# Optimization experiments

Measured on AMD Instinct MI355X. Metric: run time of the kernel, lower is better.

The kernel has to match this reference:

```python
import jax, jax.numpy as jnp
import numpy as np

U_NUM = 100000
I_NUM = 50000
D = 64
E = 4_000_000
N_LAYERS = 3


def setup_inputs() -> dict:
    key = jax.random.key(0)
    k1, k2, k3, k4 = jax.random.split(key, 4)
    return {
        "user_emb": jax.random.normal(k1, (U_NUM + 1, D), dtype=jnp.float32) * 0.1,
        "item_emb": jax.random.normal(k2, (I_NUM + 1, D), dtype=jnp.float32) * 0.1,
        "edge_user": jax.random.randint(k3, (E,), 0, U_NUM + 1, dtype=jnp.int32),
        "edge_item": jax.random.randint(k4, (E,), 0, I_NUM + 1, dtype=jnp.int32),
    }


def reference(user_emb, item_emb, edge_user, edge_item):
    U = user_emb.shape[0]
    I = item_emb.shape[0]
    N = U + I
    # Symmetrize bipartite interaction edges into full-graph COO indices.
    rows = jnp.concatenate([edge_user, edge_item + U])          # [2E]
    cols = jnp.concatenate([edge_item + U, edge_user])          # [2E]
    # Symmetric degree normalization: A_hat = D^-1/2 A D^-1/2 (deg + 1e-7)
    deg = jax.ops.segment_sum(jnp.ones(rows.shape[0], dtype=jnp.float32), rows, num_segments=N) + 1e-7
    d_inv_sqrt = deg ** -0.5
    vals = d_inv_sqrt[rows] * d_inv_sqrt[cols]                  # [2E]

    emb = jnp.concatenate([user_emb, item_emb], axis=0)         # [N, D]
    acc = emb
    x = emb
    for _ in range(N_LAYERS):
        # SpMM: x_new[r] = sum_{edges (r,c)} vals * x[c]
        x = jax.ops.segment_sum(vals[:, None] * x[cols], rows, num_segments=N)
        acc = acc + x
    total = acc / jnp.float32(N_LAYERS + 1)                     # mean over layer stack
    return total[:U], total[U:]
```

## Files before the change

kernel.cpp:

```cpp
#include <hip/hip_runtime.h>


static constexpr int D = 64;
#define BSHIFT 8
#define BROWS 256
#define KP 1024
#define TILE 2048
#define PADSLACK (7 * BROWS)

__device__ __forceinline__ float bflo(unsigned v) {
    unsigned u = v << 16;
    return __builtin_bit_cast(float, u);
}
__device__ __forceinline__ float bfhi(unsigned v) {
    unsigned u = v & 0xFFFF0000u;
    return __builtin_bit_cast(float, u);
}
__device__ __forceinline__ unsigned pack_bf16x2(float a, float b) {
    unsigned ua = __builtin_bit_cast(unsigned, a);
    unsigned ub = __builtin_bit_cast(unsigned, b);
    ua += 0x7FFFu + ((ua >> 16) & 1u);
    ub += 0x7FFFu + ((ub >> 16) & 1u);
    return (ua >> 16) | (ub & 0xFFFF0000u);
}

__global__ __launch_bounds__(256) void bucket_count(
        const int* __restrict__ eu, const int* __restrict__ ei,
        int* __restrict__ bcnt, int E, int U) {
    __shared__ int h[KP];
    int tid = threadIdx.x;
#pragma unroll
    for (int k = 0; k < 4; ++k) h[tid + k * 256] = 0;
    __syncthreads();
    int E4 = E >> 2;
    int stride = gridDim.x * blockDim.x;
    int g = blockIdx.x * blockDim.x + tid;
    const int4* eu4 = (const int4*)eu;
    const int4* ei4 = (const int4*)ei;
    for (int e = g; e < E4; e += stride) {
        int4 u = eu4[e];
        int4 it = ei4[e];
        atomicAdd(&h[u.x >> BSHIFT], 1);
        atomicAdd(&h[u.y >> BSHIFT], 1);
        atomicAdd(&h[u.z >> BSHIFT], 1);
        atomicAdd(&h[u.w >> BSHIFT], 1);
        atomicAdd(&h[(U + it.x) >> BSHIFT], 1);
        atomicAdd(&h[(U + it.y) >> BSHIFT], 1);
        atomicAdd(&h[(U + it.z) >> BSHIFT], 1);
        atomicAdd(&h[(U + it.w) >> BSHIFT], 1);
    }
    if (blockIdx.x == 0 && tid < (E - (E4 << 2))) {
        int e = (E4 << 2) + tid;
        atomicAdd(&h[eu[e] >> BSHIFT], 1);
        atomicAdd(&h[(U + ei[e]) >> BSHIFT], 1);
    }
    __syncthreads();
#pragma unroll
    for (int k = 0; k < 4; ++k) {
        int v = h[tid + k * 256];
        if (v) atomicAdd(&bcnt[tid + k * 256], v);
    }
}

__global__ void bscan(const int* __restrict__ bcnt, int* __restrict__ bbase,
                      int* __restrict__ bcursor, int KB, int twoE) {
    __shared__ int s[KP];
    int tid = threadIdx.x;
    int v = (tid < KB) ? bcnt[tid] : 0;
    s[tid] = v;
    __syncthreads();
    for (int off = 1; off < KP; off <<= 1) {
        int a = (tid >= off) ? s[tid - off] : 0;
        __syncthreads();
        s[tid] += a;
        __syncthreads();
    }
    int ex = s[tid] - v;
    if (tid < KB) { bbase[tid] = ex; bcursor[tid] = ex; }
    if (tid == KB) bbase[tid] = twoE;
    if (tid > KB) bcursor[tid] = 0;
}

__global__ __launch_bounds__(256) void bucket_scatter(
        const int* __restrict__ eu, const int* __restrict__ ei,
        int* __restrict__ bcursor, unsigned* __restrict__ pairs,
        int E, int U, int twoE) {
    __shared__ int hist[KP];
    __shared__ int sbase[KP];
    __shared__ int gbase[KP];
    __shared__ unsigned staging[TILE];
    __shared__ unsigned short sb[TILE];
    int tid = threadIdx.x;
#pragma unroll
    for (int k = 0; k < 4; ++k) hist[tid + k * 256] = 0;
    __syncthreads();
    int base_e = blockIdx.x * TILE;
    int bk[8]; unsigned pk[8];
#pragma unroll
    for (int k = 0; k < 8; ++k) {
        int e = base_e + k * 256 + tid;
        bk[k] = -1;
        if (e < twoE) {
            int r, c;
            if (e < E) { r = eu[e]; c = U + ei[e]; }
            else       { c = eu[e - E]; r = U + ei[e - E]; }
            int b = r >> BSHIFT;
            bk[k] = b;
            pk[k] = ((unsigned)(r & (BROWS - 1)) << 18) | (unsigned)c;
            atomicAdd(&hist[b], 1);
        }
    }
    __syncthreads();
    int cc[4];
#pragma unroll
    for (int k = 0; k < 4; ++k) cc[k] = hist[tid + k * 256];
    for (int off = 1; off < KP; off <<= 1) {
        int a[4];
#pragma unroll
        for (int k = 0; k < 4; ++k) {
            int idx = tid + k * 256;
            a[k] = (idx >= off) ? hist[idx - off] : 0;
        }
        __syncthreads();
#pragma unroll
        for (int k = 0; k < 4; ++k) hist[tid + k * 256] += a[k];
        __syncthreads();
    }
#pragma unroll
    for (int k = 0; k < 4; ++k) {
        int idx = tid + k * 256;
        int e0 = hist[idx] - cc[k];
        sbase[idx] = e0;
        if (cc[k] > 0) gbase[idx] = atomicAdd(&bcursor[idx], cc[k]);
        hist[idx] = e0;
    }
    __syncthreads();
#pragma unroll
    for (int k = 0; k < 8; ++k) {
        if (bk[k] >= 0) {
            int pos = atomicAdd(&hist[bk[k]], 1);
            staging[pos] = pk[k];
            sb[pos] = (unsigned short)bk[k];
        }
    }
    __syncthreads();
    int tile_n = min(TILE, twoE - base_e);
#pragma unroll
    for (int k = 0; k < 8; ++k) {
        int j = k * 256 + tid;
        if (j < tile_n) {
            int b = sb[j];
            pairs[gbase[b] + (j - sbase[b])] = staging[j];
        }
    }
}

__global__ __launch_bounds__(256) void csr_build(
        const unsigned* __restrict__ pairs, const int* __restrict__ bbase,
        int* __restrict__ deg, int* __restrict__ row_ptr, float* __restrict__ dis,
        int* __restrict__ cols, int N) {
    __shared__ int cnt[BROWS];
    __shared__ int cur[BROWS];
    __shared__ int fin[BROWS];
    int tid = threadIdx.x;
    int b = blockIdx.x;
    int lo = bbase[b], hi = bbase[b + 1];
    int cbase = lo + PADSLACK * b;
    cnt[tid] = 0;
    __syncthreads();
    for (int i = lo + tid; i < hi; i += 256) atomicAdd(&cnt[pairs[i] >> 18], 1);
    __syncthreads();
    int c = cnt[tid];
    int p = (c + 7) & ~7;
    cnt[tid] = p;
    __syncthreads();
    for (int off = 1; off < BROWS; off <<= 1) {
        int a = (tid >= off) ? cnt[tid - off] : 0;
        __syncthreads();
        cnt[tid] += a;
        __syncthreads();
    }
    int e = cnt[tid] - p;
    int r = (b << BSHIFT) + tid;
    if (r < N) {
        deg[r] = c;
        row_ptr[r] = cbase + e;
        dis[r] = rsqrtf((float)c + 1e-7f);
    }
    cur[tid] = e;
    fin[tid] = e + p;
    __syncthreads();
    for (int i = lo + tid; i < hi; i += 256) {
        unsigned pe = pairs[i];
        int pos = atomicAdd(&cur[pe >> 18], 1);
        cols[cbase + pos] = (int)(pe & 0x3FFFFu);
    }
    __syncthreads();
    for (int i = cur[tid]; i < fin[tid]; ++i) cols[cbase + i] = N;
}

__global__ __launch_bounds__(256) void init_kernel(
        const float4* __restrict__ ue4, const float4* __restrict__ ie4,
        const float* __restrict__ dis,
        uint4* __restrict__ xsA4, uint4* __restrict__ xsB4,
        float4* __restrict__ acc4, int U8, int N8) {
    int t = blockIdx.x * blockDim.x + threadIdx.x;
    if (t >= N8 + 8) return;
    if (t >= N8) {
        uint4 z = {0u, 0u, 0u, 0u};
        xsA4[t] = z;
        xsB4[t] = z;
        return;
    }
    float dv = dis[t >> 3];
    const float4* src = (t < U8) ? (ue4 + 2 * t) : (ie4 + 2 * (t - U8));
    float4 a0 = src[0];
    float4 a1 = src[1];
    acc4[2 * t] = a0;
    acc4[2 * t + 1] = a1;
    uint4 w;
    w.x = pack_bf16x2(dv * a0.x, dv * a0.y);
    w.y = pack_bf16x2(dv * a0.z, dv * a0.w);
    w.z = pack_bf16x2(dv * a1.x, dv * a1.y);
    w.w = pack_bf16x2(dv * a1.z, dv * a1.w);
    xsA4[t] = w;
}

__global__ __launch_bounds__(256) void spmm_kernel(
        const int* __restrict__ row_ptr, const int* __restrict__ deg,
        const float* __restrict__ dis, const int* __restrict__ cols,
        const unsigned* __restrict__ xs, unsigned* __restrict__ xs_next,
        float4* __restrict__ acc4, int N, float final_scale) {
    int wid = blockIdx.x * 4 + (threadIdx.x >> 6);
    if (wid >= N) return;
    int lane = threadIdx.x & 63;
    int n8 = lane >> 3;
    int dp = lane & 7;
    int start = row_ptr[wid];
    int cntp = (deg[wid] + 7) & ~7;
    float dr = dis[wid];
    const int* colp = cols + start;
    int vbase = n8 << 2;
    int dpo = dp << 2;
    float s0 = 0.f, s1 = 0.f, s2 = 0.f, s3 = 0.f;
    float s4 = 0.f, s5 = 0.f, s6 = 0.f, s7 = 0.f;
    for (int chunk = 0; chunk < cntp; chunk += 64) {
        int cv = colp[chunk + lane];
        int nq = min(64, cntp - chunk) >> 3;
        for (int q = 0; q < nq; ++q) {
            int co = __builtin_amdgcn_ds_bpermute((q << 5) + vbase, cv);
            const uint4* p = (const uint4*)(xs + (((unsigned)co) << 5) + dpo);
            uint4 v = *p;
            s0 += bflo(v.x); s1 += bfhi(v.x);
            s2 += bflo(v.y); s3 += bfhi(v.y);
            s4 += bflo(v.z); s5 += bfhi(v.z);
            s6 += bflo(v.w); s7 += bfhi(v.w);
        }
    }
#pragma unroll
    for (int m = 8; m < 64; m <<= 1) {
        s0 += __shfl_xor(s0, m); s1 += __shfl_xor(s1, m);
        s2 += __shfl_xor(s2, m); s3 += __shfl_xor(s3, m);
        s4 += __shfl_xor(s4, m); s5 += __shfl_xor(s5, m);
        s6 += __shfl_xor(s6, m); s7 += __shfl_xor(s7, m);
    }
    if (n8 == 0) {
        float x0 = dr * s0, x1 = dr * s1, x2 = dr * s2, x3 = dr * s3;
        float x4 = dr * s4, x5 = dr * s5, x6 = dr * s6, x7 = dr * s7;
        uint4 w;
        w.x = pack_bf16x2(dr * x0, dr * x1);
        w.y = pack_bf16x2(dr * x2, dr * x3);
        w.z = pack_bf16x2(dr * x4, dr * x5);
        w.w = pack_bf16x2(dr * x6, dr * x7);
        ((uint4*)xs_next)[(wid << 3) + dp] = w;
        int o = (wid << 4) + (dp << 1);
        float4 a = acc4[o];
        a.x = (a.x + x0) * final_scale;
        a.y = (a.y + x1) * final_scale;
        a.z = (a.z + x2) * final_scale;
        a.w = (a.w + x3) * final_scale;
        acc4[o] = a;
        float4 b2 = acc4[o + 1];
        b2.x = (b2.x + x4) * final_scale;
        b2.y = (b2.y + x5) * final_scale;
        b2.z = (b2.z + x6) * final_scale;
        b2.w = (b2.w + x7) * final_scale;
        acc4[o + 1] = b2;
    }
}

extern "C" void kernel_launch(void* const* d_in, const int* in_sizes, int n_in,
                              void* d_out, int out_size, void* d_ws, size_t ws_size,
                              hipStream_t stream) {
    const float* ue = (const float*)d_in[0];
    const float* ie = (const float*)d_in[1];
    const int* eu = (const int*)d_in[2];
    const int* ei = (const int*)d_in[3];
    const int U = in_sizes[0] / D;
    const int I = in_sizes[1] / D;
    const int N = U + I;
    const int E = in_sizes[2];
    const int twoE = 2 * E;
    const int KB = (N + BROWS - 1) / BROWS;
    float* out = (float*)d_out;

    char* ws = (char*)d_ws;
    auto alloc = [&](size_t bytes) {
        char* p = ws;
        ws += (bytes + 255) & ~(size_t)255;
        return p;
    };
    int* deg = (int*)alloc((size_t)N * 4);
    int* row_ptr = (int*)alloc((size_t)N * 4);
    float* dis = (float*)alloc((size_t)N * 4);
    int* bcnt = (int*)alloc(KP * 4);
    int* bbase = (int*)alloc((KP + 1) * 4);
    int* bcursor = (int*)alloc(KP * 4);
    int* cols = (int*)alloc(((size_t)twoE + (size_t)PADSLACK * (KB + 1) + 256) * 4);
    unsigned* pairs = (unsigned*)alloc((size_t)twoE * 4);
    unsigned* xsA = (unsigned*)alloc(((size_t)N + 1) * 32 * 4);
    unsigned* xsB = (unsigned*)alloc(((size_t)N + 1) * 32 * 4);

    hipMemsetAsync(bcnt, 0, KP * 4, stream);
    bucket_count<<<1024, 256, 0, stream>>>(eu, ei, bcnt, E, U);
    bscan<<<1, KP, 0, stream>>>(bcnt, bbase, bcursor, KB, twoE);
    bucket_scatter<<<(twoE + TILE - 1) / TILE, 256, 0, stream>>>(
        eu, ei, bcursor, pairs, E, U, twoE);
    csr_build<<<KB, BROWS, 0, stream>>>(pairs, bbase, deg, row_ptr, dis, cols, N);

    int N8 = N * 8, U8 = U * 8;
    init_kernel<<<(N8 + 8 + 255) / 256, 256, 0, stream>>>(
        (const float4*)ue, (const float4*)ie, dis,
        (uint4*)xsA, (uint4*)xsB, (float4*)out, U8, N8);

    unsigned* x = xsA;
    unsigned* xn = xsB;
    for (int l = 0; l < 3; ++l) {
        float fs = (l == 2) ? 0.25f : 1.0f;
        spmm_kernel<<<(N + 3) / 4, 256, 0, stream>>>(
            row_ptr, deg, dis, cols, x, xn, (float4*)out, N, fs);
        unsigned* tmp = x; x = xn; xn = tmp;
    }
}
```

Before: 668.8 us.

## Stage CSR column scatter in LDS and batch SpMM gathers for memory parallelism

csr_build now scatters column indices into a shared-memory buffer in two row halves, pads them, then writes each half to global memory contiguously instead of scattering randomly to global. The SpMM inner loop is unrolled to issue up to eight bpermutes and eight row gathers before accumulating, which raises the number of memory loads in flight. The costs are a 48KB LDS buffer that limits csr_build occupancy, extra passes over pairs and added barriers, plus more registers in the SpMM kernel.

```diff
diff --git a/kernel.cpp b/kernel.cpp
--- a/kernel.cpp
+++ b/kernel.cpp
@@ -7,6 +7,7 @@
 #define KP 1024
 #define TILE 2048
 #define PADSLACK (7 * BROWS)
+#define CSR_LDS_CAP 12288
 
 __device__ __forceinline__ float bflo(unsigned v) {
     unsigned u = v << 16;
@@ -22,6 +23,11 @@
     ua += 0x7FFFu + ((ua >> 16) & 1u);
     ub += 0x7FFFu + ((ub >> 16) & 1u);
     return (ua >> 16) | (ub & 0xFFFF0000u);
+}
+
+__device__ __forceinline__ void acc_bf2(unsigned u, float& se, float& so) {
+    se += bflo(u);
+    so += bfhi(u);
 }
 
 __global__ __launch_bounds__(256) void bucket_count(
@@ -162,6 +168,8 @@
     __shared__ int cnt[BROWS];
     __shared__ int cur[BROWS];
     __shared__ int fin[BROWS];
+    __shared__ int lbuf[CSR_LDS_CAP];
+    __shared__ int meta[2];
     int tid = threadIdx.x;
     int b = blockIdx.x;
     int lo = bbase[b], hi = bbase[b + 1];
@@ -189,14 +197,42 @@
     }
     cur[tid] = e;
     fin[tid] = e + p;
-    __syncthreads();
-    for (int i = lo + tid; i < hi; i += 256) {
-        unsigned pe = pairs[i];
-        int pos = atomicAdd(&cur[pe >> 18], 1);
-        cols[cbase + pos] = (int)(pe & 0x3FFFFu);
-    }
-    __syncthreads();
-    for (int i = cur[tid]; i < fin[tid]; ++i) cols[cbase + i] = N;
+    if (tid == 127) meta[0] = cnt[127];
+    if (tid == 255) meta[1] = cnt[255];
+    __syncthreads();
+    int half0 = meta[0];
+    int total = meta[1];
+    if (half0 <= CSR_LDS_CAP && (total - half0) <= CSR_LDS_CAP) {
+#pragma unroll
+        for (int half = 0; half < 2; ++half) {
+            int base = half ? half0 : 0;
+            int end  = half ? total : half0;
+            for (int i = lo + tid; i < hi; i += 256) {
+                unsigned pe = pairs[i];
+                int row = (int)(pe >> 18);
+                if ((row >> 7) == half) {
+                    int pos = atomicAdd(&cur[row], 1);
+                    lbuf[pos - base] = (int)(pe & 0x3FFFFu);
+                }
+            }
+            __syncthreads();
+            if ((tid >> 7) == half) {
+                for (int i = cur[tid]; i < fin[tid]; ++i) lbuf[i - base] = N;
+            }
+            __syncthreads();
+            for (int i = base + tid; i < end; i += 256)
+                cols[cbase + i] = lbuf[i - base];
+            __syncthreads();
+        }
+    } else {
+        for (int i = lo + tid; i < hi; i += 256) {
+            unsigned pe = pairs[i];
+            int pos = atomicAdd(&cur[pe >> 18], 1);
+            cols[cbase + pos] = (int)(pe & 0x3FFFFu);
+        }
+        __syncthreads();
+        for (int i = cur[tid]; i < fin[tid]; ++i) cols[cbase + i] = N;
+    }
 }
 
 __global__ __launch_bounds__(256) void init_kernel(
@@ -247,14 +283,27 @@
     for (int chunk = 0; chunk < cntp; chunk += 64) {
         int cv = colp[chunk + lane];
         int nq = min(64, cntp - chunk) >> 3;
-        for (int q = 0; q < nq; ++q) {
-            int co = __builtin_amdgcn_ds_bpermute((q << 5) + vbase, cv);
-            const uint4* p = (const uint4*)(xs + (((unsigned)co) << 5) + dpo);
-            uint4 v = *p;
-            s0 += bflo(v.x); s1 += bfhi(v.x);
-            s2 += bflo(v.y); s3 += bfhi(v.y);
-            s4 += bflo(v.z); s5 += bfhi(v.z);
-            s6 += bflo(v.w); s7 += bfhi(v.w);
+        nq = __builtin_amdgcn_readfirstlane(nq);
+        int coq[8];
+        uint4 vq[8];
+#pragma unroll
+        for (int q = 0; q < 8; ++q) {
+            if (q < nq)
+                coq[q] = __builtin_amdgcn_ds_bpermute((q << 5) + vbase, cv);
+        }
+#pragma unroll
+        for (int q = 0; q < 8; ++q) {
+            if (q < nq)
+                vq[q] = *(const uint4*)(xs + (((unsigned)coq[q]) << 5) + dpo);
+        }
+#pragma unroll
+        for (int q = 0; q < 8; ++q) {
+            if (q < nq) {
+                acc_bf2(vq[q].x, s0, s1);
+                acc_bf2(vq[q].y, s2, s3);
+                acc_bf2(vq[q].z, s4, s5);
+                acc_bf2(vq[q].w, s6, s7);
+            }
         }
     }
 #pragma unroll
```

Measured after the change: 639.1 us. 1.05x faster.
